# Kernel tuning notes

Measured on AMD Instinct MI355X. Metric: run time of the kernel, lower is better.

## Reference

```python
import jax, jax.numpy as jnp
import numpy as np

N_NODES = 100000


def gcn_conv(x, edge_index, W, b, n_nodes):
    """PyG GCNConv: add self-loops, symmetric deg^-1/2 normalization,
    linear transform, scatter-add aggregate, bias."""
    src, dst = edge_index[0], edge_index[1]
    # add self-loops
    loop = jnp.arange(n_nodes, dtype=edge_index.dtype)
    src = jnp.concatenate([src, loop])
    dst = jnp.concatenate([dst, loop])
    # transform first (in_dim >= out_dim ordering used by PyG)
    h = x @ W  # [N, out]
    # symmetric normalization from in-degree (incl. self-loops)
    ones = jnp.ones(src.shape[0], dtype=x.dtype)
    deg = jax.ops.segment_sum(ones, dst, num_segments=n_nodes)
    dinv = jnp.where(deg > 0, jax.lax.rsqrt(deg), 0.0).astype(x.dtype)
    norm = dinv[src] * dinv[dst]  # [E+N]
    msg = h[src] * norm[:, None]  # gather + scale
    out = jax.ops.segment_sum(msg, dst, num_segments=n_nodes)
    return out + b


def setup_inputs() -> dict:
    key = jax.random.key(0)
    k1, k2, k3, k4 = jax.random.split(key, 4)
    n, e = N_NODES, 1600000
    d_in, d_hid, n_cls = 256, 256, 64
    x = jax.random.normal(k1, (n, d_in), dtype=jnp.float32)
    edge_index = jax.random.randint(k2, (2, e), 0, n, dtype=jnp.int64)
    W1 = jax.random.normal(k3, (d_in, d_hid), dtype=jnp.float32) / np.sqrt(d_in)
    b1 = jnp.zeros((d_hid,), dtype=jnp.float32)
    W2 = jax.random.normal(k4, (d_hid, n_cls), dtype=jnp.float32) / np.sqrt(d_hid)
    b2 = jnp.zeros((n_cls,), dtype=jnp.float32)
    return {"x": x, "edge_index": edge_index, "W1": W1, "b1": b1, "W2": W2, "b2": b2}


def reference(x, edge_index, W1, b1, W2, b2):
    n = x.shape[0]
    h = jax.nn.relu(gcn_conv(x, edge_index, W1, b1, n))
    # dropout is identity in eval mode (training=False)
    logits = gcn_conv(h, edge_index, W2, b2, n)
    return jax.nn.log_softmax(logits, axis=1)
```

## Files before the change

### kernel.cpp

```cpp
#include <hip/hip_runtime.h>
#include <math.h>


typedef __attribute__((ext_vector_type(8))) short bf16x8;
typedef __attribute__((ext_vector_type(4))) float f32x4;

__device__ inline unsigned short f2bf(float f) {
    union { float f; unsigned int u; } v; v.f = f;
    unsigned int r = v.u + 0x7fffu + ((v.u >> 16) & 1u);
    return (unsigned short)(r >> 16);
}
__device__ inline float bf2f_lo(unsigned int u) {
    union { unsigned int u; float f; } v; v.u = u << 16; return v.f;
}
__device__ inline float bf2f_hi(unsigned int u) {
    union { unsigned int u; float f; } v; v.u = u & 0xffff0000u; return v.f;
}

__device__ inline void acc8(float* acc, uint4 q, float w) {
    acc[0] += bf2f_lo(q.x) * w; acc[1] += bf2f_hi(q.x) * w;
    acc[2] += bf2f_lo(q.y) * w; acc[3] += bf2f_hi(q.y) * w;
    acc[4] += bf2f_lo(q.z) * w; acc[5] += bf2f_hi(q.z) * w;
    acc[6] += bf2f_lo(q.w) * w; acc[7] += bf2f_hi(q.w) * w;
}

__global__ __launch_bounds__(256) void deg_rank_kernel(
    const int* __restrict__ dst, int E, int* __restrict__ cnt,
    int* __restrict__ rank) {
    int e = blockIdx.x * blockDim.x + threadIdx.x;
    if (e < E) rank[e] = atomicAdd(&cnt[dst[e]], 1);
}

__global__ __launch_bounds__(256) void scan_part1_kernel(
    const int* __restrict__ cnt, int* __restrict__ bsum, int N) {
    __shared__ int s[256];
    const int tid = threadIdx.x;
    int base = blockIdx.x * 1024 + tid * 4;
    int v = 0;
#pragma unroll
    for (int j = 0; j < 4; ++j)
        if (base + j < N) v += cnt[base + j];
    s[tid] = v;
    __syncthreads();
    for (int off = 128; off > 0; off >>= 1) {
        if (tid < off) s[tid] += s[tid + off];
        __syncthreads();
    }
    if (tid == 0) bsum[blockIdx.x] = s[0];
}

__global__ __launch_bounds__(1024) void scan_part2_kernel(
    const int* __restrict__ bsum, int* __restrict__ boffs, int NB,
    int* __restrict__ row_ptr, int N) {
    __shared__ int s[1024];
    const int tid = threadIdx.x;
    int v = (tid < NB) ? bsum[tid] : 0;
    s[tid] = v;
    __syncthreads();
    for (int off = 1; off < 1024; off <<= 1) {
        int t = (tid >= off) ? s[tid - off] : 0;
        __syncthreads();
        if (tid >= off) s[tid] += t;
        __syncthreads();
    }
    if (tid < NB) boffs[tid] = s[tid] - v;
    if (tid == 1023) row_ptr[N] = s[1023];
}

__global__ __launch_bounds__(256) void scan_part3_kernel(
    const int* __restrict__ cnt, const int* __restrict__ boffs,
    int* __restrict__ row_ptr, int N) {
    __shared__ int s[256];
    const int tid = threadIdx.x;
    int base = blockIdx.x * 1024 + tid * 4;
    int c[4];
    int v = 0;
#pragma unroll
    for (int j = 0; j < 4; ++j) {
        c[j] = (base + j < N) ? cnt[base + j] : 0;
        v += c[j];
    }
    s[tid] = v;
    __syncthreads();
    for (int off = 1; off < 256; off <<= 1) {
        int t = (tid >= off) ? s[tid - off] : 0;
        __syncthreads();
        if (tid >= off) s[tid] += t;
        __syncthreads();
    }
    int run = boffs[blockIdx.x] + s[tid] - v;
#pragma unroll
    for (int j = 0; j < 4; ++j) {
        if (base + j < N) {
            row_ptr[base + j] = run;
            run += c[j];
        }
    }
}

__global__ __launch_bounds__(256) void scatter_kernel(
    const int* __restrict__ src, const int* __restrict__ dst,
    const int* __restrict__ rank, const int* __restrict__ cnt,
    const int* __restrict__ row_ptr, int2* __restrict__ csr_ew, int E) {
    int e = blockIdx.x * blockDim.x + threadIdx.x;
    if (e >= E) return;
    int s = src[e], d = dst[e];
    float w = rsqrtf((float)cnt[s] + 1.0f) * rsqrtf((float)cnt[d] + 1.0f);
    int pos = row_ptr[d] + rank[e];
    int2 rec;
    rec.x = s;
    rec.y = __float_as_int(w);
    csr_ew[pos] = rec;
}

__global__ __launch_bounds__(256) void castw_kernel(
    const float* __restrict__ W1, const float* __restrict__ W2,
    unsigned short* __restrict__ W1t, unsigned short* __restrict__ W2t) {
    int i = blockIdx.x * 256 + threadIdx.x;
    if (i < 65536) {
        int n = i >> 8, k = i & 255;
        W1t[i] = f2bf(W1[(size_t)k * 256 + n]);
    } else if (i < 65536 + 16384) {
        int j = i - 65536;
        int n = j >> 8, k = j & 255;
        W2t[j] = f2bf(W2[(size_t)k * 64 + n]);
    }
}

__global__ __launch_bounds__(256) void gemm1_kernel(
    const float* __restrict__ A, const unsigned short* __restrict__ Bt,
    unsigned short* __restrict__ C, int M) {
    __shared__ unsigned short As[128][32];
    __shared__ unsigned short Bs[256][32];

    const int tid = threadIdx.x;
    const int wave = tid >> 6, lane = tid & 63;
    const int quad = lane >> 4, l15 = lane & 15;
    const int m0 = blockIdx.x * 128;

    f32x4 acc[8][4] = {};

    const int arow = tid >> 1;
    const int akk  = (tid & 1) << 4;
    const int gr = m0 + arow;

    for (int k0 = 0; k0 < 256; k0 += 32) {
        float4 a0 = make_float4(0.f,0.f,0.f,0.f), a1 = a0, a2 = a0, a3 = a0;
        if (gr < M) {
            const float* ap = &A[(size_t)gr * 256 + k0 + akk];
            a0 = *(const float4*)&ap[0];
            a1 = *(const float4*)&ap[4];
            a2 = *(const float4*)&ap[8];
            a3 = *(const float4*)&ap[12];
        }
        bf16x8 av0, av1;
        av0[0] = (short)f2bf(a0.x); av0[1] = (short)f2bf(a0.y);
        av0[2] = (short)f2bf(a0.z); av0[3] = (short)f2bf(a0.w);
        av0[4] = (short)f2bf(a1.x); av0[5] = (short)f2bf(a1.y);
        av0[6] = (short)f2bf(a1.z); av0[7] = (short)f2bf(a1.w);
        av1[0] = (short)f2bf(a2.x); av1[1] = (short)f2bf(a2.y);
        av1[2] = (short)f2bf(a2.z); av1[3] = (short)f2bf(a2.w);
        av1[4] = (short)f2bf(a3.x); av1[5] = (short)f2bf(a3.y);
        av1[6] = (short)f2bf(a3.z); av1[7] = (short)f2bf(a3.w);
        *(bf16x8*)&As[arow][akk]     = av0;
        *(bf16x8*)&As[arow][akk + 8] = av1;

        const unsigned short* bsrc = &Bt[(size_t)tid * 256 + k0];
        *(bf16x8*)&Bs[tid][0]  = *(const bf16x8*)&bsrc[0];
        *(bf16x8*)&Bs[tid][8]  = *(const bf16x8*)&bsrc[8];
        *(bf16x8*)&Bs[tid][16] = *(const bf16x8*)&bsrc[16];
        *(bf16x8*)&Bs[tid][24] = *(const bf16x8*)&bsrc[24];
        __syncthreads();

        bf16x8 bfv[4];
#pragma unroll
        for (int nt = 0; nt < 4; ++nt)
            bfv[nt] = *(const bf16x8*)&Bs[wave * 64 + nt * 16 + l15][quad * 8];
#pragma unroll
        for (int mt = 0; mt < 8; ++mt) {
            bf16x8 af = *(const bf16x8*)&As[mt * 16 + l15][quad * 8];
#pragma unroll
            for (int nt = 0; nt < 4; ++nt)
                acc[mt][nt] = __builtin_amdgcn_mfma_f32_16x16x32_bf16(
                    af, bfv[nt], acc[mt][nt], 0, 0, 0);
        }
        __syncthreads();
    }

#pragma unroll
    for (int mt = 0; mt < 8; ++mt) {
#pragma unroll
        for (int nt = 0; nt < 4; ++nt) {
            int gcol = wave * 64 + nt * 16 + l15;
#pragma unroll
            for (int r = 0; r < 4; ++r) {
                int grow = m0 + mt * 16 + quad * 4 + r;
                if (grow < M)
                    C[(size_t)grow * 256 + gcol] = f2bf(acc[mt][nt][r]);
            }
        }
    }
}

__global__ __launch_bounds__(256) void aggfused_kernel(
    const uint4* __restrict__ h,
    const int2* __restrict__ ew,
    const int* __restrict__ row_ptr, const int* __restrict__ cnt,
    const float* __restrict__ bias, const unsigned short* __restrict__ W2t,
    unsigned short* __restrict__ h2b, int N) {
    __shared__ unsigned short As[16][264];

    const int tid = threadIdx.x;
    const int wave = tid >> 6, lane = tid & 63;
    const int half = lane >> 5;
    const int c = lane & 31;
    const int node0 = blockIdx.x * 16;

    for (int i = 0; i < 4; ++i) {
        const int local = wave * 4 + i;
        const int node = node0 + local;
        float acc[8] = {0.f, 0.f, 0.f, 0.f, 0.f, 0.f, 0.f, 0.f};
        if (node < N) {
            float dv = rsqrtf((float)cnt[node] + 1.0f);
            float w0 = dv * dv;
            {
                uint4 q = h[(size_t)node * 32 + c];
                acc8(acc, q, half == 0 ? w0 : 0.f);
            }
            const int beg = row_ptr[node], end = row_ptr[node + 1];
            int e = beg;
            for (; e + 8 <= end; e += 8) {
                int2 r0 = ew[e + 0 + half];
                int2 r1 = ew[e + 2 + half];
                int2 r2 = ew[e + 4 + half];
                int2 r3 = ew[e + 6 + half];
                uint4 q0 = h[(size_t)r0.x * 32 + c];
                uint4 q1 = h[(size_t)r1.x * 32 + c];
                uint4 q2 = h[(size_t)r2.x * 32 + c];
                uint4 q3 = h[(size_t)r3.x * 32 + c];
                acc8(acc, q0, __int_as_float(r0.y));
                acc8(acc, q1, __int_as_float(r1.y));
                acc8(acc, q2, __int_as_float(r2.y));
                acc8(acc, q3, __int_as_float(r3.y));
            }
            for (; e < end; e += 2) {
                int idx = e + half;
                int idxc = min(idx, end - 1);
                int2 r = ew[idxc];
                float w = (idx < end) ? __int_as_float(r.y) : 0.f;
                uint4 q = h[(size_t)r.x * 32 + c];
                acc8(acc, q, w);
            }
        }
#pragma unroll
        for (int k = 0; k < 8; ++k) acc[k] += __shfl_xor(acc[k], 32, 64);

        if (half == 0) {
            float4 b0 = *(const float4*)&bias[c * 8];
            float4 b1 = *(const float4*)&bias[c * 8 + 4];
            unsigned int o0 = f2bf(fmaxf(acc[0] + b0.x, 0.f));
            unsigned int o1 = f2bf(fmaxf(acc[1] + b0.y, 0.f));
            unsigned int o2 = f2bf(fmaxf(acc[2] + b0.z, 0.f));
            unsigned int o3 = f2bf(fmaxf(acc[3] + b0.w, 0.f));
            unsigned int o4 = f2bf(fmaxf(acc[4] + b1.x, 0.f));
            unsigned int o5 = f2bf(fmaxf(acc[5] + b1.y, 0.f));
            unsigned int o6 = f2bf(fmaxf(acc[6] + b1.z, 0.f));
            unsigned int o7 = f2bf(fmaxf(acc[7] + b1.w, 0.f));
            uint4 ov;
            ov.x = o0 | (o1 << 16);
            ov.y = o2 | (o3 << 16);
            ov.z = o4 | (o5 << 16);
            ov.w = o6 | (o7 << 16);
            *(uint4*)&As[local][c * 8] = ov;
        }
    }
    __syncthreads();

    const int quad = lane >> 4, l15 = lane & 15;
    f32x4 accd = {};
#pragma unroll
    for (int k0 = 0; k0 < 8; ++k0) {
        bf16x8 af = *(const bf16x8*)&As[l15][k0 * 32 + quad * 8];
        bf16x8 bf = *(const bf16x8*)&W2t[(size_t)(wave * 16 + l15) * 256 +
                                         k0 * 32 + quad * 8];
        accd = __builtin_amdgcn_mfma_f32_16x16x32_bf16(af, bf, accd, 0, 0, 0);
    }
#pragma unroll
    for (int r = 0; r < 4; ++r) {
        int node = node0 + quad * 4 + r;
        if (node < N)
            h2b[(size_t)node * 64 + wave * 16 + l15] = f2bf(accd[r]);
    }
}

__global__ __launch_bounds__(256) void agg64_kernel(
    const uint4* __restrict__ h,
    const int2* __restrict__ ew, const int* __restrict__ row_ptr,
    const int* __restrict__ cnt, const float* __restrict__ bias,
    float* __restrict__ out, int N) {
    const int node = blockIdx.x * 4 + (threadIdx.x >> 6);
    if (node >= N) return;
    const int lane = threadIdx.x & 63;
    const int g = lane >> 3;
    const int c = lane & 7;

    float dv = rsqrtf((float)cnt[node] + 1.0f);
    float w0 = dv * dv;

    float acc[8] = {0.f, 0.f, 0.f, 0.f, 0.f, 0.f, 0.f, 0.f};
    {
        uint4 q = h[(size_t)node * 8 + c];
        acc8(acc, q, g == 0 ? w0 : 0.f);
    }

    const int beg = row_ptr[node], end = row_ptr[node + 1];
    int e = beg;
    for (; e + 16 <= end; e += 16) {
        int2 r0 = ew[e + g];
        int2 r1 = ew[e + 8 + g];
        uint4 q0 = h[(size_t)r0.x * 8 + c];
        uint4 q1 = h[(size_t)r1.x * 8 + c];
        acc8(acc, q0, __int_as_float(r0.y));
        acc8(acc, q1, __int_as_float(r1.y));
    }
    for (; e < end; e += 8) {
        int idx = e + g;
        int idxc = min(idx, end - 1);
        int2 r = ew[idxc];
        float w = (idx < end) ? __int_as_float(r.y) : 0.f;
        uint4 q = h[(size_t)r.x * 8 + c];
        acc8(acc, q, w);
    }

#pragma unroll
    for (int k = 0; k < 8; ++k) {
        acc[k] += __shfl_xor(acc[k], 8, 64);
        acc[k] += __shfl_xor(acc[k], 16, 64);
        acc[k] += __shfl_xor(acc[k], 32, 64);
    }

    float4 b0 = *(const float4*)&bias[c * 8];
    float4 b1 = *(const float4*)&bias[c * 8 + 4];
    float v[8];
    v[0] = acc[0] + b0.x; v[1] = acc[1] + b0.y;
    v[2] = acc[2] + b0.z; v[3] = acc[3] + b0.w;
    v[4] = acc[4] + b1.x; v[5] = acc[5] + b1.y;
    v[6] = acc[6] + b1.z; v[7] = acc[7] + b1.w;

    float m = v[0];
#pragma unroll
    for (int k = 1; k < 8; ++k) m = fmaxf(m, v[k]);
    m = fmaxf(m, __shfl_xor(m, 1, 64));
    m = fmaxf(m, __shfl_xor(m, 2, 64));
    m = fmaxf(m, __shfl_xor(m, 4, 64));
    float s = 0.f;
#pragma unroll
    for (int k = 0; k < 8; ++k) s += expf(v[k] - m);
    s += __shfl_xor(s, 1, 64);
    s += __shfl_xor(s, 2, 64);
    s += __shfl_xor(s, 4, 64);
    float ls = m + logf(s);

    if (g == 0) {
        float4 o0, o1;
        o0.x = v[0] - ls; o0.y = v[1] - ls; o0.z = v[2] - ls; o0.w = v[3] - ls;
        o1.x = v[4] - ls; o1.y = v[5] - ls; o1.z = v[6] - ls; o1.w = v[7] - ls;
        *(float4*)&out[(size_t)node * 64 + c * 8] = o0;
        *(float4*)&out[(size_t)node * 64 + c * 8 + 4] = o1;
    }
}

extern "C" void kernel_launch(void* const* d_in, const int* in_sizes, int n_in,
                              void* d_out, int out_size, void* d_ws, size_t ws_size,
                              hipStream_t stream) {
    const float* x  = (const float*)d_in[0];
    const int*   ei = (const int*)d_in[1];
    const float* W1 = (const float*)d_in[2];
    const float* b1 = (const float*)d_in[3];
    const float* W2 = (const float*)d_in[4];
    const float* b2 = (const float*)d_in[5];
    float* out = (float*)d_out;

    const int N = in_sizes[0] / 256;
    const int E = in_sizes[1] / 2;
    const int NP = 102400;
    const int NB = (N + 1023) / 1024;

    char* ws = (char*)d_ws;
    int*   cnt     = (int*)ws;                 ws += (size_t)NP * 4;
    int*   rank    = (int*)ws;                 ws += (size_t)E * 4;
    int*   row_ptr = (int*)ws;                 ws += (size_t)(NP + 4) * 4;
    int*   bsum    = (int*)ws;                 ws += (size_t)1024 * 4;
    int*   boffs   = (int*)ws;                 ws += (size_t)1024 * 4;
    int2*  csr_ew  = (int2*)ws;                ws += (size_t)E * 8;
    unsigned short* W1t   = (unsigned short*)ws; ws += (size_t)256 * 256 * 2;
    unsigned short* W2t   = (unsigned short*)ws; ws += (size_t)256 * 64 * 2;
    unsigned short* h1b   = (unsigned short*)ws; ws += (size_t)N * 256 * 2;
    unsigned short* h2b   = (unsigned short*)ws; ws += (size_t)N * 64 * 2;

    hipMemsetAsync(cnt, 0, (size_t)N * sizeof(int), stream);

    deg_rank_kernel<<<(E + 255) / 256, 256, 0, stream>>>(ei + E, E, cnt, rank);
    scan_part1_kernel<<<NB, 256, 0, stream>>>(cnt, bsum, N);
    scan_part2_kernel<<<1, 1024, 0, stream>>>(bsum, boffs, NB, row_ptr, N);
    scan_part3_kernel<<<NB, 256, 0, stream>>>(cnt, boffs, row_ptr, N);
    scatter_kernel<<<(E + 255) / 256, 256, 0, stream>>>(
        ei, ei + E, rank, cnt, row_ptr, csr_ew, E);

    castw_kernel<<<(65536 + 16384 + 255) / 256, 256, 0, stream>>>(W1, W2, W1t, W2t);

    gemm1_kernel<<<(N + 127) / 128, 256, 0, stream>>>(x, W1t, h1b, N);

    aggfused_kernel<<<(N + 15) / 16, 256, 0, stream>>>(
        (const uint4*)h1b, csr_ew, row_ptr, cnt, b1, W2t, h2b, N);

    agg64_kernel<<<(N + 3) / 4, 256, 0, stream>>>(
        (const uint4*)h2b, csr_ew, row_ptr, cnt, b2, out, N);
}
```

Before: 544.3 us.

## Pre-scale features by dinv, chunk layer-1 features, split aggregation from GEMM2

Edge weights are no longer stored. Both GEMMs scale their rows by deg^-1/2 before writing, and each aggregation multiplies by the destination's dinv, so the CSR holds only source indices. The per-edge rank array is replaced by a second atomic fill counter in the scatter. Layer-1 features are written in 16 column chunks of 32 bytes each, and a separate chunked aggregation kernel runs per chunk for better cache locality. GEMM2 becomes its own pass over a materialized aggregated buffer. The trade-offs are extra kernels, an extra N×256 intermediate round trip, and nondeterministic CSR order.

```diff
diff --git a/kernel.cpp b/kernel.cpp
--- a/kernel.cpp
+++ b/kernel.cpp
@@ -17,18 +17,30 @@
     union { unsigned int u; float f; } v; v.u = u & 0xffff0000u; return v.f;
 }
 
-__device__ inline void acc8(float* acc, uint4 q, float w) {
-    acc[0] += bf2f_lo(q.x) * w; acc[1] += bf2f_hi(q.x) * w;
-    acc[2] += bf2f_lo(q.y) * w; acc[3] += bf2f_hi(q.y) * w;
-    acc[4] += bf2f_lo(q.z) * w; acc[5] += bf2f_hi(q.z) * w;
-    acc[6] += bf2f_lo(q.w) * w; acc[7] += bf2f_hi(q.w) * w;
-}
-
-__global__ __launch_bounds__(256) void deg_rank_kernel(
-    const int* __restrict__ dst, int E, int* __restrict__ cnt,
-    int* __restrict__ rank) {
+__device__ inline void acc8a(float* acc, uint4 q) {
+    acc[0] += bf2f_lo(q.x); acc[1] += bf2f_hi(q.x);
+    acc[2] += bf2f_lo(q.y); acc[3] += bf2f_hi(q.y);
+    acc[4] += bf2f_lo(q.z); acc[5] += bf2f_hi(q.z);
+    acc[6] += bf2f_lo(q.w); acc[7] += bf2f_hi(q.w);
+}
+
+__global__ __launch_bounds__(256) void deg_kernel(
+    const int* __restrict__ dst, int E, int* __restrict__ cnt) {
     int e = blockIdx.x * blockDim.x + threadIdx.x;
-    if (e < E) rank[e] = atomicAdd(&cnt[dst[e]], 1);
+    if (e < E) atomicAdd(&cnt[dst[e]], 1);
+}
+
+__global__ __launch_bounds__(256) void dv_kernel(
+    const int* __restrict__ cnt, float* __restrict__ dv,
+    unsigned short* __restrict__ h1c, unsigned short* __restrict__ h2s,
+    int N) {
+    int i = blockIdx.x * 256 + threadIdx.x;
+    if (i < N) dv[i] = rsqrtf((float)cnt[i] + 1.0f);
+    if (blockIdx.x == 0) {
+        int t = threadIdx.x;
+        h1c[((size_t)(t >> 4) * (N + 1) + N) * 16 + (t & 15)] = 0;
+        if (t < 64) h2s[(size_t)N * 64 + t] = 0;
+    }
 }
 
 __global__ __launch_bounds__(256) void scan_part1_kernel(
@@ -100,17 +112,13 @@
 
 __global__ __launch_bounds__(256) void scatter_kernel(
     const int* __restrict__ src, const int* __restrict__ dst,
-    const int* __restrict__ rank, const int* __restrict__ cnt,
-    const int* __restrict__ row_ptr, int2* __restrict__ csr_ew, int E) {
+    const int* __restrict__ row_ptr, int* __restrict__ fill,
+    int* __restrict__ csr_src, int E) {
     int e = blockIdx.x * blockDim.x + threadIdx.x;
     if (e >= E) return;
-    int s = src[e], d = dst[e];
-    float w = rsqrtf((float)cnt[s] + 1.0f) * rsqrtf((float)cnt[d] + 1.0f);
-    int pos = row_ptr[d] + rank[e];
-    int2 rec;
-    rec.x = s;
-    rec.y = __float_as_int(w);
-    csr_ew[pos] = rec;
+    int d = dst[e];
+    int pos = row_ptr[d] + atomicAdd(&fill[d], 1);
+    csr_src[pos] = src[e];
 }
 
 __global__ __launch_bounds__(256) void castw_kernel(
@@ -129,7 +137,7 @@
 
 __global__ __launch_bounds__(256) void gemm1_kernel(
     const float* __restrict__ A, const unsigned short* __restrict__ Bt,
-    unsigned short* __restrict__ C, int M) {
+    const float* __restrict__ dv, unsigned short* __restrict__ C, int M) {
     __shared__ unsigned short As[128][32];
     __shared__ unsigned short Bs[256][32];
 
@@ -137,6 +145,7 @@
     const int wave = tid >> 6, lane = tid & 63;
     const int quad = lane >> 4, l15 = lane & 15;
     const int m0 = blockIdx.x * 128;
+    const size_t cstride = (size_t)(M + 1) * 16;
 
     f32x4 acc[8][4] = {};
 
@@ -190,89 +199,125 @@
 #pragma unroll
     for (int mt = 0; mt < 8; ++mt) {
 #pragma unroll
-        for (int nt = 0; nt < 4; ++nt) {
-            int gcol = wave * 64 + nt * 16 + l15;
-#pragma unroll
-            for (int r = 0; r < 4; ++r) {
-                int grow = m0 + mt * 16 + quad * 4 + r;
-                if (grow < M)
-                    C[(size_t)grow * 256 + gcol] = f2bf(acc[mt][nt][r]);
+        for (int r = 0; r < 4; ++r) {
+            int grow = m0 + mt * 16 + quad * 4 + r;
+            if (grow < M) {
+                float sc = dv[grow];
+#pragma unroll
+                for (int nt = 0; nt < 4; ++nt) {
+                    int chunk = wave * 4 + nt;
+                    C[(size_t)chunk * cstride + (size_t)grow * 16 + l15] =
+                        f2bf(acc[mt][nt][r] * sc);
+                }
             }
         }
     }
 }
 
-__global__ __launch_bounds__(256) void aggfused_kernel(
-    const uint4* __restrict__ h,
-    const int2* __restrict__ ew,
-    const int* __restrict__ row_ptr, const int* __restrict__ cnt,
-    const float* __restrict__ bias, const unsigned short* __restrict__ W2t,
-    unsigned short* __restrict__ h2b, int N) {
+__global__ __launch_bounds__(256) void aggchunk_kernel(
+    const unsigned int* __restrict__ h1c,
+    const int* __restrict__ srcs, const int* __restrict__ row_ptr,
+    const float* __restrict__ dv, const float* __restrict__ bias,
+    unsigned short* __restrict__ agg1, int N, int NBn) {
+    const int chunk = blockIdx.x / NBn;
+    const int nb    = blockIdx.x % NBn;
+    const int tid = threadIdx.x;
+    const int wave = tid >> 6, lane = tid & 63;
+    const int g = lane >> 3, c = lane & 7;
+    const unsigned int* __restrict__ hc = h1c + (size_t)chunk * (N + 1) * 8;
+    const int node0 = nb * 16 + wave * 4;
+
+    int bg[4], en[4];
+#pragma unroll
+    for (int n = 0; n < 4; ++n) {
+        int node = node0 + n;
+        bool ok = node < N;
+        bg[n] = ok ? row_ptr[node] : 0;
+        en[n] = ok ? row_ptr[node + 1] : 0;
+    }
+
+    const int sn = g & 3;
+    const int snode = node0 + sn;
+    int ssrc = (g < 4 && snode < N) ? snode : N;
+    unsigned int qs = hc[(size_t)ssrc * 8 + c];
+    float a0[4], a1[4];
+#pragma unroll
+    for (int n = 0; n < 4; ++n) {
+        a0[n] = (sn == n) ? bf2f_lo(qs) : 0.f;
+        a1[n] = (sn == n) ? bf2f_hi(qs) : 0.f;
+    }
+
+    int T = 0;
+#pragma unroll
+    for (int n = 0; n < 4; ++n) T = max(T, (en[n] - bg[n] + 7) >> 3);
+
+    if (T > 0) {
+        int pos[4], rc[4];
+#pragma unroll
+        for (int n = 0; n < 4; ++n) {
+            pos[n] = bg[n] + g;
+            int cl = max(min(pos[n], en[n] - 1), 0);
+            int ld = __builtin_nontemporal_load(&srcs[cl]);
+            rc[n] = (pos[n] < en[n]) ? ld : N;
+        }
+        for (int it = 0; it < T; ++it) {
+            unsigned int q0 = hc[(size_t)rc[0] * 8 + c];
+            unsigned int q1 = hc[(size_t)rc[1] * 8 + c];
+            unsigned int q2 = hc[(size_t)rc[2] * 8 + c];
+            unsigned int q3 = hc[(size_t)rc[3] * 8 + c];
+#pragma unroll
+            for (int n = 0; n < 4; ++n) {
+                pos[n] += 8;
+                int cl = max(min(pos[n], en[n] - 1), 0);
+                int ld = __builtin_nontemporal_load(&srcs[cl]);
+                rc[n] = (pos[n] < en[n]) ? ld : N;
+            }
+            a0[0] += bf2f_lo(q0); a1[0] += bf2f_hi(q0);
+            a0[1] += bf2f_lo(q1); a1[1] += bf2f_hi(q1);
+            a0[2] += bf2f_lo(q2); a1[2] += bf2f_hi(q2);
+            a0[3] += bf2f_lo(q3); a1[3] += bf2f_hi(q3);
+        }
+    }
+
+#pragma unroll
+    for (int n = 0; n < 4; ++n) {
+        a0[n] += __shfl_xor(a0[n], 8, 64);  a1[n] += __shfl_xor(a1[n], 8, 64);
+        a0[n] += __shfl_xor(a0[n], 16, 64); a1[n] += __shfl_xor(a1[n], 16, 64);
+        a0[n] += __shfl_xor(a0[n], 32, 64); a1[n] += __shfl_xor(a1[n], 32, 64);
+    }
+
+    if (g < 4 && snode < N) {
+        float r0 = (sn == 0) ? a0[0] : (sn == 1) ? a0[1] : (sn == 2) ? a0[2] : a0[3];
+        float r1 = (sn == 0) ? a1[0] : (sn == 1) ? a1[1] : (sn == 2) ? a1[2] : a1[3];
+        float dvd = dv[snode];
+        int f = chunk * 16 + c * 2;
+        float v0 = fmaxf(r0 * dvd + bias[f], 0.f);
+        float v1 = fmaxf(r1 * dvd + bias[f + 1], 0.f);
+        unsigned int o = (unsigned int)f2bf(v0) | ((unsigned int)f2bf(v1) << 16);
+        *(unsigned int*)&agg1[(size_t)snode * 256 + f] = o;
+    }
+}
+
+__global__ __launch_bounds__(256) void gemm2_kernel(
+    const uint4* __restrict__ A,
+    const unsigned short* __restrict__ W2t,
+    const float* __restrict__ dv,
+    unsigned short* __restrict__ h2s, int N) {
     __shared__ unsigned short As[16][264];
-
     const int tid = threadIdx.x;
     const int wave = tid >> 6, lane = tid & 63;
-    const int half = lane >> 5;
-    const int c = lane & 31;
     const int node0 = blockIdx.x * 16;
 
-    for (int i = 0; i < 4; ++i) {
-        const int local = wave * 4 + i;
-        const int node = node0 + local;
-        float acc[8] = {0.f, 0.f, 0.f, 0.f, 0.f, 0.f, 0.f, 0.f};
+    {
+        int r = tid >> 4, q = tid & 15;
+        int node = node0 + r;
+        uint4 v0 = {0, 0, 0, 0}, v1 = v0;
         if (node < N) {
-            float dv = rsqrtf((float)cnt[node] + 1.0f);
-            float w0 = dv * dv;
-            {
-                uint4 q = h[(size_t)node * 32 + c];
-                acc8(acc, q, half == 0 ? w0 : 0.f);
-            }
-            const int beg = row_ptr[node], end = row_ptr[node + 1];
-            int e = beg;
-            for (; e + 8 <= end; e += 8) {
-                int2 r0 = ew[e + 0 + half];
-                int2 r1 = ew[e + 2 + half];
-                int2 r2 = ew[e + 4 + half];
-                int2 r3 = ew[e + 6 + half];
-                uint4 q0 = h[(size_t)r0.x * 32 + c];
-                uint4 q1 = h[(size_t)r1.x * 32 + c];
-                uint4 q2 = h[(size_t)r2.x * 32 + c];
-                uint4 q3 = h[(size_t)r3.x * 32 + c];
-                acc8(acc, q0, __int_as_float(r0.y));
-                acc8(acc, q1, __int_as_float(r1.y));
-                acc8(acc, q2, __int_as_float(r2.y));
-                acc8(acc, q3, __int_as_float(r3.y));
-            }
-            for (; e < end; e += 2) {
-                int idx = e + half;
-                int idxc = min(idx, end - 1);
-                int2 r = ew[idxc];
-                float w = (idx < end) ? __int_as_float(r.y) : 0.f;
-                uint4 q = h[(size_t)r.x * 32 + c];
-                acc8(acc, q, w);
-            }
-        }
-#pragma unroll
-        for (int k = 0; k < 8; ++k) acc[k] += __shfl_xor(acc[k], 32, 64);
-
-        if (half == 0) {
-            float4 b0 = *(const float4*)&bias[c * 8];
-            float4 b1 = *(const float4*)&bias[c * 8 + 4];
-            unsigned int o0 = f2bf(fmaxf(acc[0] + b0.x, 0.f));
-            unsigned int o1 = f2bf(fmaxf(acc[1] + b0.y, 0.f));
-            unsigned int o2 = f2bf(fmaxf(acc[2] + b0.z, 0.f));
-            unsigned int o3 = f2bf(fmaxf(acc[3] + b0.w, 0.f));
-            unsigned int o4 = f2bf(fmaxf(acc[4] + b1.x, 0.f));
-            unsigned int o5 = f2bf(fmaxf(acc[5] + b1.y, 0.f));
-            unsigned int o6 = f2bf(fmaxf(acc[6] + b1.z, 0.f));
-            unsigned int o7 = f2bf(fmaxf(acc[7] + b1.w, 0.f));
-            uint4 ov;
-            ov.x = o0 | (o1 << 16);
-            ov.y = o2 | (o3 << 16);
-            ov.z = o4 | (o5 << 16);
-            ov.w = o6 | (o7 << 16);
-            *(uint4*)&As[local][c * 8] = ov;
-        }
+            v0 = A[(size_t)node * 32 + q * 2];
+            v1 = A[(size_t)node * 32 + q * 2 + 1];
+        }
+        *(uint4*)&As[r][q * 16]     = v0;
+        *(uint4*)&As[r][q * 16 + 8] = v1;
     }
     __syncthreads();
 
@@ -289,14 +334,15 @@
     for (int r = 0; r < 4; ++r) {
         int node = node0 + quad * 4 + r;
         if (node < N)
-            h2b[(size_t)node * 64 + wave * 16 + l15] = f2bf(accd[r]);
+            h2s[(size_t)node * 64 + wave * 16 + l15] =
+                f2bf(accd[r] * dv[node]);
     }
 }
 
 __global__ __launch_bounds__(256) void agg64_kernel(
     const uint4* __restrict__ h,
-    const int2* __restrict__ ew, const int* __restrict__ row_ptr,
-    const int* __restrict__ cnt, const float* __restrict__ bias,
+    const int* __restrict__ srcs, const int* __restrict__ row_ptr,
+    const float* __restrict__ dv, const float* __restrict__ bias,
     float* __restrict__ out, int N) {
     const int node = blockIdx.x * 4 + (threadIdx.x >> 6);
     if (node >= N) return;
@@ -304,32 +350,33 @@
     const int g = lane >> 3;
     const int c = lane & 7;
 
-    float dv = rsqrtf((float)cnt[node] + 1.0f);
-    float w0 = dv * dv;
-
     float acc[8] = {0.f, 0.f, 0.f, 0.f, 0.f, 0.f, 0.f, 0.f};
     {
-        uint4 q = h[(size_t)node * 8 + c];
-        acc8(acc, q, g == 0 ? w0 : 0.f);
+        int ss = (g == 0) ? node : N;
+        uint4 q = h[(size_t)ss * 8 + c];
+        acc8a(acc, q);
     }
 
     const int beg = row_ptr[node], end = row_ptr[node + 1];
-    int e = beg;
-    for (; e + 16 <= end; e += 16) {
-        int2 r0 = ew[e + g];
-        int2 r1 = ew[e + 8 + g];
-        uint4 q0 = h[(size_t)r0.x * 8 + c];
-        uint4 q1 = h[(size_t)r1.x * 8 + c];
-        acc8(acc, q0, __int_as_float(r0.y));
-        acc8(acc, q1, __int_as_float(r1.y));
-    }
-    for (; e < end; e += 8) {
-        int idx = e + g;
-        int idxc = min(idx, end - 1);
-        int2 r = ew[idxc];
-        float w = (idx < end) ? __int_as_float(r.y) : 0.f;
-        uint4 q = h[(size_t)r.x * 8 + c];
-        acc8(acc, q, w);
+    if (beg < end) {
+        int p0 = beg + g, p1 = beg + 8 + g;
+        int cl0 = max(min(p0, end - 1), 0), cl1 = max(min(p1, end - 1), 0);
+        int l0 = __builtin_nontemporal_load(&srcs[cl0]);
+        int l1 = __builtin_nontemporal_load(&srcs[cl1]);
+        int r0 = (p0 < end) ? l0 : N;
+        int r1 = (p1 < end) ? l1 : N;
+        for (int e = beg; e < end; e += 16) {
+            uint4 q0 = h[(size_t)r0 * 8 + c];
+            uint4 q1 = h[(size_t)r1 * 8 + c];
+            p0 += 16; p1 += 16;
+            cl0 = max(min(p0, end - 1), 0); cl1 = max(min(p1, end - 1), 0);
+            l0 = __builtin_nontemporal_load(&srcs[cl0]);
+            l1 = __builtin_nontemporal_load(&srcs[cl1]);
+            acc8a(acc, q0);
+            acc8a(acc, q1);
+            r0 = (p0 < end) ? l0 : N;
+            r1 = (p1 < end) ? l1 : N;
+        }
     }
 
 #pragma unroll
@@ -339,13 +386,14 @@
         acc[k] += __shfl_xor(acc[k], 32, 64);
     }
 
+    float dvd = dv[node];
     float4 b0 = *(const float4*)&bias[c * 8];
     float4 b1 = *(const float4*)&bias[c * 8 + 4];
     float v[8];
-    v[0] = acc[0] + b0.x; v[1] = acc[1] + b0.y;
-    v[2] = acc[2] + b0.z; v[3] = acc[3] + b0.w;
-    v[4] = acc[4] + b1.x; v[5] = acc[5] + b1.y;
-    v[6] = acc[6] + b1.z; v[7] = acc[7] + b1.w;
+    v[0] = acc[0] * dvd + b0.x; v[1] = acc[1] * dvd + b0.y;
+    v[2] = acc[2] * dvd + b0.z; v[3] = acc[3] * dvd + b0.w;
+    v[4] = acc[4] * dvd + b1.x; v[5] = acc[5] * dvd + b1.y;
+    v[6] = acc[6] * dvd + b1.z; v[7] = acc[7] * dvd + b1.w;
 
     float m = v[0];
 #pragma unroll
@@ -385,35 +433,42 @@
     const int E = in_sizes[1] / 2;
     const int NP = 102400;
     const int NB = (N + 1023) / 1024;
+    const int NBn = (N + 15) / 16;
 
     char* ws = (char*)d_ws;
     int*   cnt     = (int*)ws;                 ws += (size_t)NP * 4;
-    int*   rank    = (int*)ws;                 ws += (size_t)E * 4;
+    int*   fill    = (int*)ws;                 ws += (size_t)NP * 4;
     int*   row_ptr = (int*)ws;                 ws += (size_t)(NP + 4) * 4;
     int*   bsum    = (int*)ws;                 ws += (size_t)1024 * 4;
     int*   boffs   = (int*)ws;                 ws += (size_t)1024 * 4;
-    int2*  csr_ew  = (int2*)ws;                ws += (size_t)E * 8;
-    unsigned short* W1t   = (unsigned short*)ws; ws += (size_t)256 * 256 * 2;
-    unsigned short* W2t   = (unsigned short*)ws; ws += (size_t)256 * 64 * 2;
-    unsigned short* h1b   = (unsigned short*)ws; ws += (size_t)N * 256 * 2;
-    unsigned short* h2b   = (unsigned short*)ws; ws += (size_t)N * 64 * 2;
-
-    hipMemsetAsync(cnt, 0, (size_t)N * sizeof(int), stream);
-
-    deg_rank_kernel<<<(E + 255) / 256, 256, 0, stream>>>(ei + E, E, cnt, rank);
+    int*   csr_src = (int*)ws;                 ws += (size_t)(E + 8) * 4;
+    unsigned short* W1t = (unsigned short*)ws; ws += (size_t)256 * 256 * 2;
+    unsigned short* W2t = (unsigned short*)ws; ws += (size_t)256 * 64 * 2;
+    float* dv = (float*)ws;                    ws += (size_t)NP * 4;
+    unsigned short* h1c  = (unsigned short*)ws; ws += (size_t)16 * (N + 1) * 16 * 2;
+    unsigned short* agg1 = (unsigned short*)ws; ws += (size_t)N * 256 * 2;
+    unsigned short* h2s  = (unsigned short*)ws; ws += (size_t)(N + 1) * 64 * 2;
+
+    hipMemsetAsync(cnt, 0, (size_t)2 * NP * sizeof(int), stream);
+
+    deg_kernel<<<(E + 255) / 256, 256, 0, stream>>>(ei + E, E, cnt);
+    dv_kernel<<<(N + 255) / 256, 256, 0, stream>>>(cnt, dv, h1c, h2s, N);
     scan_part1_kernel<<<NB, 256, 0, stream>>>(cnt, bsum, N);
     scan_part2_kernel<<<1, 1024, 0, stream>>>(bsum, boffs, NB, row_ptr, N);
     scan_part3_kernel<<<NB, 256, 0, stream>>>(cnt, boffs, row_ptr, N);
     scatter_kernel<<<(E + 255) / 256, 256, 0, stream>>>(
-        ei, ei + E, rank, cnt, row_ptr, csr_ew, E);
+        ei, ei + E, row_ptr, fill, csr_src, E);
 
     castw_kernel<<<(65536 + 16384 + 255) / 256, 256, 0, stream>>>(W1, W2, W1t, W2t);
 
-    gemm1_kernel<<<(N + 127) / 128, 256, 0, stream>>>(x, W1t, h1b, N);
-
-    aggfused_kernel<<<(N + 15) / 16, 256, 0, stream>>>(
-        (const uint4*)h1b, csr_ew, row_ptr, cnt, b1, W2t, h2b, N);
+    gemm1_kernel<<<(N + 127) / 128, 256, 0, stream>>>(x, W1t, dv, h1c, N);
+
+    aggchunk_kernel<<<16 * NBn, 256, 0, stream>>>(
+        (const unsigned int*)h1c, csr_src, row_ptr, dv, b1, agg1, N, NBn);
+
+    gemm2_kernel<<<(N + 15) / 16, 256, 0, stream>>>(
+        (const uint4*)agg1, W2t, dv, h2s, N);
 
     agg64_kernel<<<(N + 3) / 4, 256, 0, stream>>>(
-        (const uint4*)h2b, csr_ew, row_ptr, cnt, b2, out, N);
-}
+        (const uint4*)h2s, csr_src, row_ptr, dv, b2, out, N);
+}
```

Result: slower. 832.1 us (+52.9%).
